# Kernel tuning notes

Measured on AMD Instinct MI355X. Metric: run time of the kernel, lower is better.

The kernel has to match this reference:

```python
import jax, jax.numpy as jnp
import numpy as np

N = 160000   # active voxels
C = 64       # embed_channels
K = 2048     # clusters per level
G = 128      # voxel grid side (grid_size)
NEG = 0.01   # LeakyReLU negative slope (torch default)
EPS_BN = 1e-5


def _build_neighbors():
    # Random unique active voxels in a G^3 grid; 27-neighborhood index map for SubMConv3d.
    rng = np.random.default_rng(0)
    codes = np.sort(rng.choice(G ** 3, size=N, replace=False))
    xc = codes // (G * G); yc = (codes // G) % G; zc = codes % G
    nbrs = []
    for dx in (-1, 0, 1):
        for dy in (-1, 0, 1):
            for dz in (-1, 0, 1):
                nx, ny, nz = xc + dx, yc + dy, zc + dz
                inb = (nx >= 0) & (nx < G) & (ny >= 0) & (ny < G) & (nz >= 0) & (nz < G)
                ncode = nx * (G * G) + ny * G + nz
                pos = np.searchsorted(codes, np.where(inb, ncode, 0))
                pos = np.clip(pos, 0, N - 1)
                found = inb & (codes[pos] == ncode)
                nbrs.append(np.where(found, pos, -1))
    return np.stack(nbrs).astype(np.int32)  # [27, N], -1 = no active neighbor


def setup_inputs():
    key = jax.random.key(0)
    def nrm(i, shape, s=0.05):
        return jax.random.normal(jax.random.fold_in(key, i), shape, jnp.float32) * s
    return {
        'feat': jax.random.normal(jax.random.fold_in(key, 0), (N, C), jnp.float32),
        'lw_W': nrm(1, (3, C, C)), 'lw_g': jnp.ones((3, C)), 'lw_b': jnp.zeros((3, C)),
        'w_W': nrm(2, (3, C, C)),
        'proj_W': nrm(3, (4, C, C)), 'proj_g': jnp.ones((4, C)), 'proj_b': jnp.zeros((4, C)),
        'adaptive_W': nrm(4, (C, 3)),
        'fuse_W': nrm(5, (2 * C, C)), 'fuse_g': jnp.ones((C,)), 'fuse_b': jnp.zeros((C,)),
        'conv1_W': nrm(6, (27, C, C)), 'bn1_g': jnp.ones((C,)), 'bn1_b': jnp.zeros((C,)),
        'conv2_W': nrm(7, (27, C, C)), 'bn2_g': jnp.ones((C,)), 'bn2_b': jnp.zeros((C,)),
        'clusters': jax.random.randint(jax.random.fold_in(key, 8), (3, N), 0, K, dtype=jnp.int32),
        'nbr': jnp.asarray(_build_neighbors()),
    }


def _bn(x, g, b):
    # BatchNorm1d, training-mode (biased batch stats over N)
    m = x.mean(0)
    v = x.var(0)
    return (x - m) * jax.lax.rsqrt(v + EPS_BN) * g + b


def _lrelu(x):
    return jax.nn.leaky_relu(x, NEG)


def _seg_sum(x, seg):
    return jax.ops.segment_sum(x, seg, num_segments=K)


def _subm_conv(f, nbr, W):
    # Submanifold 3x3x3 conv: per kernel offset, masked gather + [C,C] matmul.
    out = jnp.zeros((f.shape[0], W.shape[-1]), f.dtype)
    for k in range(27):
        idx = nbr[k]
        g = jnp.where((idx >= 0)[:, None], f[jnp.maximum(idx, 0)], 0.0)
        out = out + g @ W[k]
    return out


def reference(feat, lw_W, lw_g, lw_b, w_W, proj_W, proj_g, proj_b, adaptive_W,
              fuse_W, fuse_g, fuse_b, conv1_W, bn1_g, bn1_b, conv2_W, bn2_g, bn2_b,
              clusters, nbr):
    feats = []
    for i in range(3):  # depth-1 cluster levels
        c = clusters[i]
        cnt = jnp.clip(_seg_sum(jnp.ones((feat.shape[0], 1), feat.dtype), c), 1.0, None)
        pw = _lrelu(_bn(feat @ lw_W[i], lw_g[i], lw_b[i]))
        pw = pw - (_seg_sum(pw, c) / cnt)[c]          # center by cluster mean
        pw = pw @ w_W[i]
        pw = jnp.exp(pw - pw.max())                    # global-max-stabilized exp
        pw = pw / (_seg_sum(pw, c)[c] + 1e-6)          # per-cluster softmax
        pfeat = _lrelu(_bn(feat @ proj_W[i], proj_g[i], proj_b[i])) * pw
        feats.append(_seg_sum(pfeat, c)[c])            # pool then broadcast back
    adp = jax.nn.softmax(feat @ adaptive_W, axis=1)    # [N, 3]
    feats = jnp.stack(feats, axis=1)                   # [N, 3, C]
    feats = jnp.einsum('ln,lnc->lc', adp, feats)
    f = _lrelu(_bn(feat @ proj_W[3], proj_g[3], proj_b[3]))
    f = jnp.concatenate([f, feats], axis=1)
    f = _lrelu(_bn(f @ fuse_W, fuse_g, fuse_b)) + feat
    res = f
    v = _lrelu(_bn(_subm_conv(f, nbr, conv1_W), bn1_g, bn1_b))
    v = _bn(_subm_conv(v, nbr, conv2_W), bn2_g, bn2_b)
    return _lrelu(v + res)
```

## Files before the change

### kernel.cpp

```cpp
#include <hip/hip_runtime.h>
#include <hip/hip_bf16.h>
#include <math.h>

#define KCL 2048
#define LRELU_NEG 0.01f
#define EPSBN 1e-5f
#define OSTR 72

using s8v = __attribute__((ext_vector_type(8))) short;
using f4v = __attribute__((ext_vector_type(4))) float;

union U8 { ushort u[8]; uint4 v; };

__device__ __forceinline__ float lrelu(float x) { return x > 0.f ? x : LRELU_NEG * x; }
__device__ __forceinline__ ushort f2bf(float f) {
    __hip_bfloat16 h = __float2bfloat16(f);
    return *reinterpret_cast<ushort*>(&h);
}
__device__ __forceinline__ float bf2f(ushort u) { return __uint_as_float(((unsigned)u) << 16); }

__device__ __forceinline__ unsigned encf(float f) {
    unsigned u = __float_as_uint(f);
    return (u & 0x80000000u) ? ~u : (u | 0x80000000u);
}
// ... 19 lines not shown
__device__ __forceinline__ void mfma_tileG(const uint4* As, const ushort* Wmat, int ws, int koff,
                                           int rowA0, int rowA1, int swA0, int swA1,
                                           int l15, int lg, f4v acc[2][4]) {
    const s8v* Av = (const s8v*)As;
#pragma unroll
    for (int kb = 0; kb < 2; ++kb) {
        int gch = kb * 4 + lg;
        s8v a0 = Av[rowA0 * 8 + (gch ^ swA0)];
        s8v a1 = Av[rowA1 * 8 + (gch ^ swA1)];
#pragma unroll
        for (int nf = 0; nf < 4; ++nf) {
            int col = nf * 16 + l15;
            s8v bf = *(const s8v*)(Wmat + (size_t)col * ws + koff + gch * 8);
            acc[0][nf] = __builtin_amdgcn_mfma_f32_16x16x32_bf16(a0, bf, acc[0][nf], 0, 0, 0);
            acc[1][nf] = __builtin_amdgcn_mfma_f32_16x16x32_bf16(a1, bf, acc[1][nf], 0, 0, 0);
        }
    }
}

__device__ __forceinline__ void stage_a_bf16(const ushort* S, uint4* As, int row, int n, int arow, int ah) {
    uint4 c0 = {0, 0, 0, 0}, c1 = c0, c2 = c0, c3 = c0;
    if (row < n) {
        const uint4* s = (const uint4*)(S + (size_t)row * 64) + ah * 4;
        c0 = s[0]; c1 = s[1]; c2 = s[2]; c3 = s[3];
    }
    int sw = arow & 7;
    uint4* dst = As + arow * 8;
    dst[(ah * 4 + 0) ^ sw] = c0;
    dst[(ah * 4 + 1) ^ sw] = c1;
    dst[(ah * 4 + 2) ^ sw] = c2;
    dst[(ah * 4 + 3) ^ sw] = c3;
}

__device__ __forceinline__ void stage_a_vals(const float* vals, uint4* As, int arow, int ah) {
    int sw = arow & 7;
    uint4* dst = As + arow * 8;
#pragma unroll
    for (int c = 0; c < 4; ++c) {
        U8 u;
#pragma unroll
        for (int e = 0; e < 8; ++e) u.u[e] = f2bf(vals[c * 8 + e]);
        dst[(ah * 4 + c) ^ sw] = u.v;
    }
}

__device__ __forceinline__ void tile_to_ost(const f4v acc[2][4], ushort* ost, int w, int lane) {
    const int l15 = lane & 15, lg = lane >> 4;
#pragma unroll
    for (int rf = 0; rf < 2; ++rf)
#pragma unroll
        for (int nf = 0; nf < 4; ++nf)
#pragma unroll
            for (int q = 0; q < 4; ++q)
                ost[(w * 32 + rf * 16 + lg * 4 + q) * OSTR + nf * 16 + l15] = f2bf(acc[rf][nf][q]);
}

__device__ __forceinline__ void ost_store(const ushort* ost, ushort* out, int n, int rb, int arow, int ah) {
    int row = rb + arow;
    if (row < n) {
        uint4* dst = (uint4*)(out + (size_t)row * 64 + ah * 32);
        const uint4* src = (const uint4*)(ost + arow * OSTR + ah * 32);
        dst[0] = src[0]; dst[1] = src[1]; dst[2] = src[2]; dst[3] = src[3];
    }
}

__device__ __forceinline__ void tile_stats(const f4v acc[2][4], float* red, double* statp,
                                           int n, int rb, int w, int lane, int t) {
    const int l15 = lane & 15, lg = lane >> 4;
    int base = rb + w * 32;
#pragma unroll
    for (int nf = 0; nf < 4; ++nf) {
        float s = 0.f, s2 = 0.f;
#pragma unroll
        for (int rf = 0; rf < 2; ++rf)
#pragma unroll
            for (int q = 0; q < 4; ++q) {
                int r = base + rf * 16 + lg * 4 + q;
                if (r < n) {
                    float v = acc[rf][nf][q];
                    s += v;
                    s2 += v * v;
                }
            }
        s += __shfl_xor(s, 16); s += __shfl_xor(s, 32);
        s2 += __shfl_xor(s2, 16); s2 += __shfl_xor(s2, 32);
        if (lg == 0) {
            red[w * 64 + nf * 16 + l15] = s;
// ... 89 lines not shown
    int t = threadIdx.x;
    int base = t * 8;
    int v[8];
    int s = 0;
#pragma unroll
    for (int j = 0; j < 8; ++j) { v[j] = c[base + j]; s += v[j]; }
    part[t] = s;
    __syncthreads();
    if (t == 0) {
        int acc = 0;
        for (int i = 0; i < 256; ++i) { pref[i] = acc; acc += part[i]; }
    }
    __syncthreads();
    int acc = pref[t] + l * n;
#pragma unroll
    for (int j = 0; j < 8; ++j) {
        off[l * KCL + base + j] = acc;
        cursor[l * KCL + base + j] = acc;
        acc += v[j];
    }
}

__global__ __launch_bounds__(256) void scatter_kernel(const int* __restrict__ clusters, int* __restrict__ cursor,
                                                      int* __restrict__ perm, int n) {
    long n3 = (long)n * 3;
    for (long i = (long)blockIdx.x * 256 + threadIdx.x; i < n3; i += (long)gridDim.x * 256) {
        int l = (i >= n) + (i >= 2 * (long)n);
        int c = clusters[i];
        int pos = atomicAdd(&cursor[l * KCL + c], 1);
        perm[pos] = (int)(i - (long)l * n);
    }
}

__device__ __forceinline__ void mega_one(const uint4* As, float* red, ushort* ost, const ushort* Wmat,
                                         ushort* out, double* statp, int n, int rb, int w, int lane,
                                         int arow, int ah, int t) {
    const int l15 = lane & 15, lg = lane >> 4;
    int rowA0 = w * 32 + l15, rowA1 = rowA0 + 16;
    f4v acc[2][4];
#pragma unroll
    for (int rf = 0; rf < 2; ++rf)
#pragma unroll
        for (int nf = 0; nf < 4; ++nf)
#pragma unroll
            for (int q = 0; q < 4; ++q) acc[rf][nf][q] = 0.f;
    mfma_tileG(As, Wmat, 64, 0, rowA0, rowA1, rowA0 & 7, rowA1 & 7, l15, lg, acc);
    tile_to_ost(acc, ost, w, lane);
    tile_stats(acc, red, statp, n, rb, w, lane, t);
    __syncthreads();
    ost_store(ost, out, n, rb, arow, ah);
    tile_stats_final(red, statp, t);
    __syncthreads();
}

__global__ __launch_bounds__(256) void mega7_gemm(const ushort* __restrict__ feat16,
                                                  const ushort* __restrict__ wt64,
                                                  ushort* __restrict__ o0, ushort* __restrict__ o1,
                                                  ushort* __restrict__ o2, ushort* __restrict__ o3,
                                                  ushort* __restrict__ o4, ushort* __restrict__ o5,
                                                  ushort* __restrict__ o6,
                                                  int n, double* __restrict__ stats) {
    __shared__ uint4 As[128 * 8];
    __shared__ float red[512];
    __shared__ ushort ost[128 * OSTR];
    int t = threadIdx.x, lane = t & 63, w = t >> 6;
    int rb = blockIdx.x * 128;
    int arow = t >> 1, ah = t & 1;
    stage_a_bf16(feat16, As, rb + arow, n, arow, ah);
    __syncthreads();
    mega_one(As, red, ost, wt64 + (size_t)0 * 4096, o0, stats + 0 * 128, n, rb, w, lane, arow, ah, t);
    mega_one(As, red, ost, wt64 + (size_t)1 * 4096, o1, stats + 2 * 128, n, rb, w, lane, arow, ah, t);
    mega_one(As, red, ost, wt64 + (size_t)2 * 4096, o2, stats + 4 * 128, n, rb, w, lane, arow, ah, t);
    mega_one(As, red, ost, wt64 + (size_t)6 * 4096, o3, stats + 1 * 128, n, rb, w, lane, arow, ah, t);
    mega_one(As, red, ost, wt64 + (size_t)7 * 4096, o4, stats + 3 * 128, n, rb, w, lane, arow, ah, t);
    mega_one(As, red, ost, wt64 + (size_t)8 * 4096, o5, stats + 5 * 128, n, rb, w, lane, arow, ah, t);
    mega_one(As, red, ost, wt64 + (size_t)9 * 4096, o6, stats + 6 * 128, n, rb, w, lane, arow, ah, t);
}

__global__ __launch_bounds__(256) void reduce_mean3_kernel(const ushort* __restrict__ A3,
                                                           const double* __restrict__ stats,
                                                           const float* __restrict__ lw_g,
                                                           const float* __restrict__ lw_b, int n,
                                                           const int* __restrict__ cnts, const int* __restrict__ offs,
                                                           const int* __restrict__ perm,
                                                           float* __restrict__ meanB3) {
    int l = blockIdx.x >> 11, c = blockIdx.x & (KCL - 1);
    const ushort* A = A3 + (size_t)l * n * 64;
    __shared__ float sb[128];
    bn_sb(stats + (size_t)(2 * l) * 128, lw_g + l * 64, lw_b + l * 64, n, sb);
    int t = threadIdx.x, col = t & 63, rg = t >> 6;
    int o = offs[l * KCL + c], m = cnts[l * KCL + c];
    float acc = 0.f;
    float sc = sb[col], bi = sb[64 + col];
    for (int j = rg; j < m; j += 4) {
        int row = perm[o + j];
        acc += lrelu(bf2f(A[(size_t)row * 64 + col]) * sc + bi);
    }
    __shared__ float red[256];
    red[t] = acc;
    __syncthreads();
    if (t < 64) {
        float s = red[t] + red[t + 64] + red[t + 128] + red[t + 192];
        float cf = (float)m;
        if (cf < 1.f) cf = 1.f;
        meanB3[(size_t)l * KCL * 64 + (size_t)c * 64 + col] = s / cf;
    }
}

__global__ __launch_bounds__(256) void mw3_gemm(const float* __restrict__ meanB3, const ushort* __restrict__ wW16,
                                                float* __restrict__ MW3) {
    __shared__ uint4 As[128 * 8];
    int l = blockIdx.x >> 4, b = blockIdx.x & 15;
    const float* src = meanB3 + (size_t)l * KCL * 64;
    float* out = MW3 + (size_t)l * KCL * 64;
    int t = threadIdx.x, lane = t & 63, w = t >> 6;
    int rb = b * 128;
    int arow = t >> 1, ah = t & 1;
    const int l15 = lane & 15, lg = lane >> 4;
    {
        float vals[32];
        const float4* s = (const float4*)(src + (size_t)(rb + arow) * 64 + ah * 32);
#pragma unroll
        for (int q = 0; q < 8; ++q) {
            float4 x = s[q];
            vals[q * 4 + 0] = x.x; vals[q * 4 + 1] = x.y;
            vals[q * 4 + 2] = x.z; vals[q * 4 + 3] = x.w;
        }
        stage_a_vals(vals, As, arow, ah);
    }
    __syncthreads();
    f4v acc[2][4];
#pragma unroll
    for (int rf = 0; rf < 2; ++rf)
#pragma unroll
        for (int nf = 0; nf < 4; ++nf)
#pragma unroll
            for (int q = 0; q < 4; ++q) acc[rf][nf][q] = 0.f;
    int rowA0 = w * 32 + l15, rowA1 = rowA0 + 16;
    mfma_tileG(As, wW16 + (size_t)l * 4096, 64, 0, rowA0, rowA1, rowA0 & 7, rowA1 & 7, l15, lg, acc);
    int base = rb + w * 32;
#pragma unroll
    for (int rf = 0; rf < 2; ++rf)
#pragma unroll
        for (int nf = 0; nf < 4; ++nf)
#pragma unroll
            for (int q = 0; q < 4; ++q) {
                int r = base + rf * 16 + lg * 4 + q;
                out[(size_t)r * 64 + nf * 16 + l15] = acc[rf][nf][q];
            }
}

__global__ __launch_bounds__(256) void cgemm3(ushort* __restrict__ A3io, const ushort* __restrict__ wW16,
                                              const float* __restrict__ MW3, const int* __restrict__ clusters,
                                              const double* __restrict__ stats, const float* __restrict__ lw_g,
                                              const float* __restrict__ lw_b,
                                              unsigned* __restrict__ gmax, int n, int nb) {
    __shared__ uint4 As[128 * 8];
    __shared__ float sb[128];
    __shared__ ushort ost[128 * OSTR];
    int l = blockIdx.x / nb, b = blockIdx.x % nb;
    ushort* A = A3io + (size_t)l * n * 64;
    const float* MW = MW3 + (size_t)l * KCL * 64;
    const int* clus = clusters + (size_t)l * n;
    int t = threadIdx.x, lane = t & 63, w = t >> 6;
    int rb = b * 128;
    int arow = t >> 1, ah = t & 1;
    const int l15 = lane & 15, lg = lane >> 4;

    bn_sb(stats + (size_t)(2 * l) * 128, lw_g + l * 64, lw_b + l * 64, n, sb);
    {
        int row = rb + arow;
        float vals[32];
        if (row < n) {
            const U8* s8p = (const U8*)(A + (size_t)row * 64 + ah * 32);
#pragma unroll
            for (int c = 0; c < 4; ++c) {
                U8 u = s8p[c];
#pragma unroll
                for (int e = 0; e < 8; ++e) {
                    int col = ah * 32 + c * 8 + e;
                    vals[c * 8 + e] = lrelu(bf2f(u.u[e]) * sb[col] + sb[64 + col]);
                }
            }
        } else {
#pragma unroll
            for (int i = 0; i < 32; ++i) vals[i] = 0.f;
        }
        stage_a_vals(vals, As, arow, ah);
    }
    __syncthreads();
    f4v acc[2][4];
#pragma unroll
    for (int rf = 0; rf < 2; ++rf)
#pragma unroll
        for (int nf = 0; nf < 4; ++nf)
#pragma unroll
            for (int q = 0; q < 4; ++q) acc[rf][nf][q] = 0.f;
    int rowA0 = w * 32 + l15, rowA1 = rowA0 + 16;
    mfma_tileG(As, wW16 + (size_t)l * 4096, 64, 0, rowA0, rowA1, rowA0 & 7, rowA1 & 7, l15, lg, acc);
    int base = rb + w * 32;
    float m = -INFINITY;
#pragma unroll
    for (int rf = 0; rf < 2; ++rf)
#pragma unroll
        for (int q = 0; q < 4; ++q) {
            int r = base + rf * 16 + lg * 4 + q;
            int c = (r < n) ? clus[r] : 0;
            const float* mwr = MW + (size_t)c * 64;
            int orow = (w * 32 + rf * 16 + lg * 4 + q) * OSTR;
#pragma unroll
            for (int nf = 0; nf < 4; ++nf) {
                int col = nf * 16 + l15;
                float v = acc[rf][nf][q] - mwr[col];
                ost[orow + col] = f2bf(v);
                if (r < n) m = fmaxf(m, v);
            }
        }
    float* sp = (float*)As;
    sp[t] = m;
    __syncthreads();
    ost_store(ost, A, n, rb, arow, ah);
    for (int s = 128; s > 0; s >>= 1) {
        if (t < s) sp[t] = fmaxf(sp[t], sp[t + s]);
        __syncthreads();
    }
    if (t == 0) atomicMax(&gmax[l], encf(sp[0]));
}

__global__ __launch_bounds__(256) void expf3_kernel(const ushort* __restrict__ C3, const ushort* __restrict__ E0,
                                                    const ushort* __restrict__ E1, const ushort* __restrict__ E2,
                                                    const double* __restrict__ stats,
                                                    const float* __restrict__ proj_g, const float* __restrict__ proj_b,
                                                    int n, const unsigned* __restrict__ gmax,
                                                    const int* __restrict__ cnts, const int* __restrict__ offs,
                                                    const int* __restrict__ perm, float* __restrict__ seg3) {
    int l = blockIdx.x >> 11, c = blockIdx.x & (KCL - 1);
    const ushort* C = C3 + (size_t)l * n * 64;
    const ushort* E = (l == 0) ? E0 : (l == 1) ? E1 : E2;
    __shared__ float sb[128];
    bn_sb(stats + (size_t)(2 * l + 1) * 128, proj_g + l * 64, proj_b + l * 64, n, sb);
    int t = threadIdx.x, col = t & 63, rg = t >> 6;
    float gm = decf(gmax[l]);
    int o = offs[l * KCL + c], m = cnts[l * KCL + c];
    float accd = 0.f, accn = 0.f;
    float sc = sb[col], bi = sb[64 + col];
    for (int j = rg; j < m; j += 4) {
        int row = perm[o + j];
        float d = expf(bf2f(C[(size_t)row * 64 + col]) - gm);
        float pf = lrelu(bf2f(E[(size_t)row * 64 + col]) * sc + bi);
        accd += d;
        accn += pf * d;
    }
    __shared__ float redd[256], redn[256];
    redd[t] = accd;
    redn[t] = accn;
    __syncthreads();
    if (t < 64) {
        float sd = redd[t] + redd[t + 64] + redd[t + 128] + redd[t + 192];
        float sn = redn[t] + redn[t + 64] + redn[t + 128] + redn[t + 192];
        seg3[(size_t)l * KCL * 64 + (size_t)c * 64 + col] = sn / (sd + 1e-6f);
    }
}

__global__ __launch_bounds__(256) void fuse_mfma(const ushort* __restrict__ P3, const double* __restrict__ statsP,
                                                 const float* __restrict__ gg, const float* __restrict__ bb, int n,
                                                 const float* __restrict__ adp, const int* __restrict__ clusters,
                                                 const float* __restrict__ s3_0, const float* __restrict__ s3_1,
                                                 const float* __restrict__ s3_2, const ushort* __restrict__ WfT,
                                                 ushort* __restrict__ out, double* __restrict__ stats_out) {
    __shared__ uint4 As[128 * 8];
    __shared__ float sb[128];
    __shared__ ushort ost[128 * OSTR];
    int t = threadIdx.x, lane = t & 63, w = t >> 6;
    int rb = blockIdx.x * 128;
    int arow = t >> 1, ah = t & 1;
    const int l15 = lane & 15, lg = lane >> 4;

    bn_sb(statsP, gg, bb, n, sb);

    f4v acc[2][4];
#pragma unroll
    for (int rf = 0; rf < 2; ++rf)
#pragma unroll
        for (int nf = 0; nf < 4; ++nf)
#pragma unroll
            for (int q = 0; q < 4; ++q) acc[rf][nf][q] = 0.f;

    int rowA0 = w * 32 + l15, rowA1 = rowA0 + 16;
    int row = rb + arow;

    for (int p = 0; p < 2; ++p) {
        if (p) __syncthreads();
        float vals[32];
        if (row < n) {
            if (p == 0) {
                const U8* s8p = (const U8*)(P3 + (size_t)row * 64 + ah * 32);
#pragma unroll
                for (int c = 0; c < 4; ++c) {
                    U8 u = s8p[c];
#pragma unroll
                    for (int e = 0; e < 8; ++e) {
                        int col = ah * 32 + c * 8 + e;
                        vals[c * 8 + e] = lrelu(bf2f(u.u[e]) * sb[col] + sb[64 + col]);
                    }
                }
            } else {
                float a0 = adp[(size_t)row * 3 + 0], a1 = adp[(size_t)row * 3 + 1], a2 = adp[(size_t)row * 3 + 2];
                const float* r0 = s3_0 + (size_t)clusters[row] * 64 + ah * 32;
                const float* r1 = s3_1 + (size_t)clusters[(size_t)n + row] * 64 + ah * 32;
                const float* r2 = s3_2 + (size_t)clusters[2 * (size_t)n + row] * 64 + ah * 32;
#pragma unroll
                for (int i = 0; i < 32; ++i) vals[i] = a0 * r0[i] + a1 * r1[i] + a2 * r2[i];
            }
        } else {
#pragma unroll
            for (int i = 0; i < 32; ++i) vals[i] = 0.f;
        }
        stage_a_vals(vals, As, arow, ah);
        __syncthreads();
        mfma_tileG(As, WfT, 128, p * 64, rowA0, rowA1, rowA0 & 7, rowA1 & 7, l15, lg, acc);
    }
    tile_to_ost(acc, ost, w, lane);
    float* red = (float*)As;
    tile_stats(acc, red, stats_out, n, rb, w, lane, t);
    __syncthreads();
    ost_store(ost, out, n, rb, arow, ah);
    tile_stats_final(red, stats_out, t);
}

__global__ __launch_bounds__(256) void subm_conv_db(const ushort* __restrict__ fin, const int* __restrict__ nbr,
                                                    const ushort* __restrict__ Wt, ushort* __restrict__ vout,
                                                    int n, double* __restrict__ stats_out) {
    __shared__ uint4 As[2][128 * 8];
    __shared__ uint4 Ws[2][64 * 8];
    int t = threadIdx.x;
    int lane = t & 63, w = t >> 6;
    int rb = blockIdx.x * 128;
    int arow = t >> 1, ah = t & 1;
    int wrow = t >> 2, wq = t & 3;
    const int l15 = lane & 15, lg = lane >> 4;
    int rowA0 = w * 32 + l15, rowA1 = rowA0 + 16;
    int swA0 = rowA0 & 7, swA1 = rowA1 & 7;
    const bool rowok = (rb + arow) < n;
    const int swa = arow & 7, sww = wrow & 7;

    f4v acc[2][4];
#pragma unroll
    for (int rf = 0; rf < 2; ++rf)
#pragma unroll
        for (int nf = 0; nf < 4; ++nf)
#pragma unroll
            for (int q = 0; q < 4; ++q) acc[rf][nf][q] = 0.f;

    bool fc0, fc1, wzc, wzn = false;
    {
        int gi = rowok ? nbr[rb + arow] : -1;
// ... 54 lines not shown
                    s8v av0 = Av[rowA0 * 8 + (gch ^ swA0)];
#pragma unroll
                    for (int nf = 0; nf < 4; ++nf)
                        acc[0][nf] = __builtin_amdgcn_mfma_f32_16x16x32_bf16(av0, bfr[nf], acc[0][nf], 0, 0, 0);
                }
                if (fc1) {
                    s8v av1 = Av[rowA1 * 8 + (gch ^ swA1)];
#pragma unroll
                    for (int nf = 0; nf < 4; ++nf)
                        acc[1][nf] = __builtin_amdgcn_mfma_f32_16x16x32_bf16(av1, bfr[nf], acc[1][nf], 0, 0, 0);
                }
            }
        }
        if (k < 26) {
            if (!(missn && wzn)) {
                uint4* dst = As[cur ^ 1] + arow * 8;
                dst[(ah * 4 + 0) ^ swa] = a0;
                dst[(ah * 4 + 1) ^ swa] = a1;
                dst[(ah * 4 + 2) ^ swa] = a2;
                dst[(ah * 4 + 3) ^ swa] = a3;
            }
            uint4* wdst = Ws[cur ^ 1] + wrow * 8;
            wdst[wq ^ sww] = w0;
            wdst[(wq + 4) ^ sww] = w1;
            cur ^= 1;
            bool nw = wzc;
            wzc = missn;
            wzn = nw;
            fc0 = fn0;
            fc1 = fn1;
        }
    }
    __syncthreads();
    ushort* ost = (ushort*)As;
    float* red = (float*)Ws;
    tile_to_ost(acc, ost, w, lane);
    tile_stats(acc, red, stats_out, n, rb, w, lane, t);
    __syncthreads();
    ost_store(ost, vout, n, rb, arow, ah);
    tile_stats_final(red, stats_out, t);
}

__global__ __launch_bounds__(256) void addfeat_kernel(const ushort* __restrict__ t3, const double* __restrict__ stats,
                                                      const float* __restrict__ g, const float* __restrict__ b,
                                                      const float* __restrict__ feat, ushort* __restrict__ f16,
                                                      int n) {
    __shared__ float sb[128];
    bn_sb(stats, g, b, n, sb);
    long total4 = (long)n * 16;
    for (long i = (long)blockIdx.x * 256 + threadIdx.x; i < total4; i += (long)gridDim.x * 256) {
        int c0 = (int)(i & 15) * 4;
        ushort4 xv = ((const ushort4*)t3)[i];
        float4 fz = ((const float4*)feat)[i];
        ushort4 u;
        u.x = f2bf(lrelu(bf2f(xv.x) * sb[c0 + 0] + sb[64 + c0 + 0]) + fz.x);
        u.y = f2bf(lrelu(bf2f(xv.y) * sb[c0 + 1] + sb[64 + c0 + 1]) + fz.y);
        u.z = f2bf(lrelu(bf2f(xv.z) * sb[c0 + 2] + sb[64 + c0 + 2]) + fz.z);
        u.w = f2bf(lrelu(bf2f(xv.w) * sb[c0 + 3] + sb[64 + c0 + 3]) + fz.w);
        ((ushort4*)f16)[i] = u;
    }
}

__global__ __launch_bounds__(256) void bnlrelu_tobf16_kernel(const ushort* __restrict__ v,
                                                             const double* __restrict__ stats,
                                                             const float* __restrict__ g, const float* __restrict__ b,
                                                             ushort* __restrict__ o16, int n) {
    __shared__ float sb[128];
    bn_sb(stats, g, b, n, sb);
// ... 66 lines not shown
    size_t stats_off = alloc((size_t)10 * 128 * 8);
    size_t gmax_off = alloc(16);
    size_t zbytes = off;
    size_t offs_off = alloc((size_t)3 * KCL * 4);
    size_t cur_off = alloc((size_t)3 * KCL * 4);
    size_t perm_off = alloc((size_t)3 * n * 4);
    size_t mean_off = alloc((size_t)3 * KCL * 64 * 4);
    size_t mw_off = alloc((size_t)3 * KCL * 64 * 4);
    size_t seg3_off = alloc((size_t)3 * KCL * 64 * 4);
    size_t adp_off = alloc((size_t)n * 3 * 4);
    size_t feat16_off = alloc((size_t)n * 64 * 2);
    size_t ra_off = alloc((size_t)3 * n * 64 * 2);
    size_t re_off = alloc((size_t)2 * n * 64 * 2);
    size_t wt64_off = alloc((size_t)64 * 4096 * 2);
    size_t wfT_off = alloc((size_t)8192 * 2);

    int* cnts = (int*)(ws + cnt_off);
    double* stats = (double*)(ws + stats_off);
    unsigned* gmax = (unsigned*)(ws + gmax_off);
    int* offs = (int*)(ws + offs_off);
    int* cursor = (int*)(ws + cur_off);
    int* perm = (int*)(ws + perm_off);
    float* meanB3 = (float*)(ws + mean_off);
    float* MW3 = (float*)(ws + mw_off);
    float* seg3 = (float*)(ws + seg3_off);
    float* adp = (float*)(ws + adp_off);
    ushort* feat16 = (ushort*)(ws + feat16_off);
    ushort* RA = (ushort*)(ws + ra_off);
    ushort* RE = (ushort*)(ws + re_off);
    ushort* wt64 = (ushort*)(ws + wt64_off);
    ushort* wfT = (ushort*)(ws + wfT_off);
    float* outp = (float*)d_out;

    ushort* A3 = RA;
    ushort* E0 = RE;
    ushort* E1 = RE + (size_t)n * 64;
    ushort* E2 = (ushort*)d_out;
    ushort* P3 = (ushort*)d_out + (size_t)n * 64;
    ushort* t3buf = RA;
    ushort* fbuf16 = RA + (size_t)n * 64;
    ushort* c1out = RA + (size_t)2 * n * 64;
    ushort* cbuf = RE;
    ushort* c2out = RE + (size_t)n * 64;

    const ushort* wW16 = wt64 + (size_t)3 * 4096;
    const ushort* conv1W16 = wt64 + (size_t)10 * 4096;
    const ushort* conv2W16 = wt64 + (size_t)37 * 4096;

    hipMemsetAsync(d_ws, 0, zbytes, stream);

    const int GEMM_BLK = (n + 127) / 128;
    const int EW_BLK = 2048;

    prep_wt64<<<64, 256, 0, stream>>>(lw_W, w_W, proj_W, conv1_W, conv2_W, wt64);
    prep_fuse<<<1, 256, 0, stream>>>(fuse_W, wfT);
    adp_cvt_kernel<<<1024, 256, 0, stream>>>(feat, adaptive_W, adp, feat16, n);

    hist3_kernel<<<384, 256, 0, stream>>>(clusters, cnts, n);
    scan_kernel<<<3, 256, 0, stream>>>(cnts, offs, cursor, n);
    scatter_kernel<<<1024, 256, 0, stream>>>(clusters, cursor, perm, n);

    mega7_gemm<<<GEMM_BLK, 256, 0, stream>>>(feat16, wt64,
                                             A3, A3 + (size_t)n * 64, A3 + (size_t)2 * n * 64,
                                             E0, E1, E2, P3, n, stats);
    reduce_mean3_kernel<<<3 * KCL, 256, 0, stream>>>(A3, stats, lw_g, lw_b, n, cnts, offs, perm, meanB3);
    mw3_gemm<<<3 * 16, 256, 0, stream>>>(meanB3, wW16, MW3);
    cgemm3<<<3 * GEMM_BLK, 256, 0, stream>>>(A3, wW16, MW3, clusters, stats, lw_g, lw_b, gmax, n, GEMM_BLK);
    expf3_kernel<<<3 * KCL, 256, 0, stream>>>(A3, E0, E1, E2, stats, proj_g, proj_b, n, gmax,
                                              cnts, offs, perm, seg3);

    fuse_mfma<<<GEMM_BLK, 256, 0, stream>>>(P3, stats + 6 * 128, proj_g + 192, proj_b + 192, n,
                                            adp, clusters,
                                            seg3, seg3 + (size_t)KCL * 64, seg3 + (size_t)2 * KCL * 64,
                                            wfT, t3buf, stats + 7 * 128);
    addfeat_kernel<<<EW_BLK, 256, 0, stream>>>(t3buf, stats + 7 * 128, fuse_g, fuse_b, feat, fbuf16, n);

    subm_conv_db<<<GEMM_BLK, 256, 0, stream>>>(fbuf16, nbr, conv1W16, c1out, n, stats + 8 * 128);
    bnlrelu_tobf16_kernel<<<EW_BLK, 256, 0, stream>>>(c1out, stats + 8 * 128, bn1_g, bn1_b, cbuf, n);

    subm_conv_db<<<GEMM_BLK, 256, 0, stream>>>(cbuf, nbr, conv2W16, c2out, n, stats + 9 * 128);
    final_kernel<<<EW_BLK, 256, 0, stream>>>(c2out, stats + 9 * 128, bn2_g, bn2_b, fbuf16, outp, n);
}
```

Baseline: 589.6 us.

## Recompute projection GEMMs on the fly instead of materializing seven intermediate tensors

The first GEMM kernel now only accumulates batch-norm statistics for the seven projections and no longer writes the bf16 outputs. Every downstream kernel (cluster mean, global max, per-cluster softmax/pool, fuse) recomputes its projection from feat16 with MFMA, gathering rows via the cluster permutation where needed. This removes large intermediate writes and reads to global memory, at the cost of redundant matrix multiplies and extra shared-memory staging in the cluster-gather kernels.

```diff
diff --git a/kernel.cpp b/kernel.cpp
--- a/kernel.cpp
+++ b/kernel.cpp
@@ -75,6 +75,20 @@
     dst[(ah * 4 + 3) ^ sw] = c3;
 }
 
+__device__ __forceinline__ void stage_a_gather(const ushort* S, uint4* As, int gi, int arow, int ah) {
+    uint4 c0 = {0, 0, 0, 0}, c1 = c0, c2 = c0, c3 = c0;
+    if (gi >= 0) {
+        const uint4* s = (const uint4*)(S + (size_t)gi * 64) + ah * 4;
+        c0 = s[0]; c1 = s[1]; c2 = s[2]; c3 = s[3];
+    }
+    int sw = arow & 7;
+    uint4* dst = As + arow * 8;
+    dst[(ah * 4 + 0) ^ sw] = c0;
+    dst[(ah * 4 + 1) ^ sw] = c1;
+    dst[(ah * 4 + 2) ^ sw] = c2;
+    dst[(ah * 4 + 3) ^ sw] = c3;
+}
+
 __device__ __forceinline__ void stage_a_vals(const float* vals, uint4* As, int arow, int ah) {
     int sw = arow & 7;
     uint4* dst = As + arow * 8;
@@ -96,6 +110,17 @@
 #pragma unroll
             for (int q = 0; q < 4; ++q)
                 ost[(w * 32 + rf * 16 + lg * 4 + q) * OSTR + nf * 16 + l15] = f2bf(acc[rf][nf][q]);
+}
+
+__device__ __forceinline__ void ost_read_row(const ushort* ost, int arow, int ah, float* vals) {
+    const uint4* src = (const uint4*)(ost + arow * OSTR + ah * 32);
+#pragma unroll
+    for (int c = 0; c < 4; ++c) {
+        U8 u;
+        u.v = src[c];
+#pragma unroll
+        for (int e = 0; e < 8; ++e) vals[c * 8 + e] = bf2f(u.u[e]);
+    }
 }
 
 __device__ __forceinline__ void ost_store(const ushort* ost, ushort* out, int n, int rb, int arow, int ah) {
@@ -251,78 +276,96 @@
     }
 }
 
-__device__ __forceinline__ void mega_one(const uint4* As, float* red, ushort* ost, const ushort* Wmat,
-                                         ushort* out, double* statp, int n, int rb, int w, int lane,
-                                         int arow, int ah, int t) {
-    const int l15 = lane & 15, lg = lane >> 4;
-    int rowA0 = w * 32 + l15, rowA1 = rowA0 + 16;
-    f4v acc[2][4];
-#pragma unroll
-    for (int rf = 0; rf < 2; ++rf)
-#pragma unroll
-        for (int nf = 0; nf < 4; ++nf)
-#pragma unroll
-            for (int q = 0; q < 4; ++q) acc[rf][nf][q] = 0.f;
-    mfma_tileG(As, Wmat, 64, 0, rowA0, rowA1, rowA0 & 7, rowA1 & 7, l15, lg, acc);
-    tile_to_ost(acc, ost, w, lane);
-    tile_stats(acc, red, statp, n, rb, w, lane, t);
-    __syncthreads();
-    ost_store(ost, out, n, rb, arow, ah);
-    tile_stats_final(red, statp, t);
-    __syncthreads();
-}
-
-__global__ __launch_bounds__(256) void mega7_gemm(const ushort* __restrict__ feat16,
-                                                  const ushort* __restrict__ wt64,
-                                                  ushort* __restrict__ o0, ushort* __restrict__ o1,
-                                                  ushort* __restrict__ o2, ushort* __restrict__ o3,
-                                                  ushort* __restrict__ o4, ushort* __restrict__ o5,
-                                                  ushort* __restrict__ o6,
-                                                  int n, double* __restrict__ stats) {
+__global__ __launch_bounds__(256) void stats7_gemm(const ushort* __restrict__ feat16,
+                                                   const ushort* __restrict__ wt64,
+                                                   int n, double* __restrict__ stats) {
     __shared__ uint4 As[128 * 8];
     __shared__ float red[512];
-    __shared__ ushort ost[128 * OSTR];
     int t = threadIdx.x, lane = t & 63, w = t >> 6;
     int rb = blockIdx.x * 128;
     int arow = t >> 1, ah = t & 1;
+    const int l15 = lane & 15, lg = lane >> 4;
+    int rowA0 = w * 32 + l15, rowA1 = rowA0 + 16;
     stage_a_bf16(feat16, As, rb + arow, n, arow, ah);
     __syncthreads();
-    mega_one(As, red, ost, wt64 + (size_t)0 * 4096, o0, stats + 0 * 128, n, rb, w, lane, arow, ah, t);
-    mega_one(As, red, ost, wt64 + (size_t)1 * 4096, o1, stats + 2 * 128, n, rb, w, lane, arow, ah, t);
-    mega_one(As, red, ost, wt64 + (size_t)2 * 4096, o2, stats + 4 * 128, n, rb, w, lane, arow, ah, t);
-    mega_one(As, red, ost, wt64 + (size_t)6 * 4096, o3, stats + 1 * 128, n, rb, w, lane, arow, ah, t);
-    mega_one(As, red, ost, wt64 + (size_t)7 * 4096, o4, stats + 3 * 128, n, rb, w, lane, arow, ah, t);
-    mega_one(As, red, ost, wt64 + (size_t)8 * 4096, o5, stats + 5 * 128, n, rb, w, lane, arow, ah, t);
-    mega_one(As, red, ost, wt64 + (size_t)9 * 4096, o6, stats + 6 * 128, n, rb, w, lane, arow, ah, t);
-}
-
-__global__ __launch_bounds__(256) void reduce_mean3_kernel(const ushort* __restrict__ A3,
-                                                           const double* __restrict__ stats,
-                                                           const float* __restrict__ lw_g,
-                                                           const float* __restrict__ lw_b, int n,
-                                                           const int* __restrict__ cnts, const int* __restrict__ offs,
-                                                           const int* __restrict__ perm,
-                                                           float* __restrict__ meanB3) {
+    const int wsl[7] = {0, 1, 2, 6, 7, 8, 9};
+    const int ssl[7] = {0, 2, 4, 1, 3, 5, 6};
+#pragma unroll
+    for (int p = 0; p < 7; ++p) {
+        f4v acc[2][4];
+#pragma unroll
+        for (int rf = 0; rf < 2; ++rf)
+#pragma unroll
+            for (int nf = 0; nf < 4; ++nf)
+#pragma unroll
+                for (int q = 0; q < 4; ++q) acc[rf][nf][q] = 0.f;
+        mfma_tileG(As, wt64 + (size_t)wsl[p] * 4096, 64, 0, rowA0, rowA1, rowA0 & 7, rowA1 & 7,
+                   l15, lg, acc);
+        tile_stats(acc, red, stats + (size_t)ssl[p] * 128, n, rb, w, lane, t);
+        __syncthreads();
+        tile_stats_final(red, stats + (size_t)ssl[p] * 128, t);
+        __syncthreads();
+    }
+}
+
+__global__ __launch_bounds__(256) void mean3_fused(const ushort* __restrict__ feat16,
+                                                   const ushort* __restrict__ wt64,
+                                                   const double* __restrict__ stats,
+                                                   const float* __restrict__ lw_g, const float* __restrict__ lw_b,
+                                                   int n, const int* __restrict__ cnts,
+                                                   const int* __restrict__ offs, const int* __restrict__ perm,
+                                                   float* __restrict__ meanB3) {
     int l = blockIdx.x >> 11, c = blockIdx.x & (KCL - 1);
-    const ushort* A = A3 + (size_t)l * n * 64;
     __shared__ float sb[128];
+    __shared__ uint4 As[128 * 8];
+    __shared__ float red[256];
     bn_sb(stats + (size_t)(2 * l) * 128, lw_g + l * 64, lw_b + l * 64, n, sb);
-    int t = threadIdx.x, col = t & 63, rg = t >> 6;
+    int t = threadIdx.x, lane = t & 63, w = t >> 6;
+    int arow = t >> 1, ah = t & 1;
+    const int l15 = lane & 15, lg = lane >> 4;
+    int rowA0 = w * 32 + l15, rowA1 = rowA0 + 16;
+    const ushort* Wm = wt64 + (size_t)l * 4096;
     int o = offs[l * KCL + c], m = cnts[l * KCL + c];
-    float acc = 0.f;
-    float sc = sb[col], bi = sb[64 + col];
-    for (int j = rg; j < m; j += 4) {
-        int row = perm[o + j];
-        acc += lrelu(bf2f(A[(size_t)row * 64 + col]) * sc + bi);
-    }
-    __shared__ float red[256];
-    red[t] = acc;
+    float colsum[4] = {0.f, 0.f, 0.f, 0.f};
+    for (int ch = 0; ch < m; ch += 128) {
+        int j = ch + arow;
+        int gi = (j < m) ? perm[o + j] : -1;
+        __syncthreads();
+        stage_a_gather(feat16, As, gi, arow, ah);
+        __syncthreads();
+        f4v acc[2][4];
+#pragma unroll
+        for (int rf = 0; rf < 2; ++rf)
+#pragma unroll
+            for (int nf = 0; nf < 4; ++nf)
+#pragma unroll
+                for (int q = 0; q < 4; ++q) acc[rf][nf][q] = 0.f;
+        mfma_tileG(As, Wm, 64, 0, rowA0, rowA1, rowA0 & 7, rowA1 & 7, l15, lg, acc);
+#pragma unroll
+        for (int rf = 0; rf < 2; ++rf)
+#pragma unroll
+            for (int q = 0; q < 4; ++q) {
+                int jr = ch + w * 32 + rf * 16 + lg * 4 + q;
+                if (jr < m)
+#pragma unroll
+                    for (int nf = 0; nf < 4; ++nf) {
+                        int col = nf * 16 + l15;
+                        colsum[nf] += lrelu(acc[rf][nf][q] * sb[col] + sb[64 + col]);
+                    }
+            }
+    }
+#pragma unroll
+    for (int nf = 0; nf < 4; ++nf) {
+        float s = colsum[nf];
+        s += __shfl_xor(s, 16); s += __shfl_xor(s, 32);
+        if (lg == 0) red[w * 64 + nf * 16 + l15] = s;
+    }
     __syncthreads();
     if (t < 64) {
-        float s = red[t] + red[t + 64] + red[t + 128] + red[t + 192];
+        float s = red[t] + red[64 + t] + red[128 + t] + red[192 + t];
         float cf = (float)m;
         if (cf < 1.f) cf = 1.f;
-        meanB3[(size_t)l * KCL * 64 + (size_t)c * 64 + col] = s / cf;
+        meanB3[((size_t)l * KCL + c) * 64 + t] = s / cf;
     }
 }
 
@@ -369,76 +412,77 @@
             }
 }
 
-__global__ __launch_bounds__(256) void cgemm3(ushort* __restrict__ A3io, const ushort* __restrict__ wW16,
-                                              const float* __restrict__ MW3, const int* __restrict__ clusters,
-                                              const double* __restrict__ stats, const float* __restrict__ lw_g,
-                                              const float* __restrict__ lw_b,
-                                              unsigned* __restrict__ gmax, int n, int nb) {
+__global__ __launch_bounds__(256) void gmax3_kernel(const ushort* __restrict__ feat16,
+                                                    const ushort* __restrict__ wt64,
+                                                    const float* __restrict__ MW3,
+                                                    const int* __restrict__ clusters,
+                                                    const double* __restrict__ stats,
+                                                    const float* __restrict__ lw_g, const float* __restrict__ lw_b,
+                                                    unsigned* __restrict__ gmax, int n, int nb) {
+    __shared__ float sb[128];
     __shared__ uint4 As[128 * 8];
-    __shared__ float sb[128];
+    __shared__ uint4 As2[128 * 8];
     __shared__ ushort ost[128 * OSTR];
+    __shared__ float sp[256];
     int l = blockIdx.x / nb, b = blockIdx.x % nb;
-    ushort* A = A3io + (size_t)l * n * 64;
-    const float* MW = MW3 + (size_t)l * KCL * 64;
-    const int* clus = clusters + (size_t)l * n;
+    int rb = b * 128;
+    bn_sb(stats + (size_t)(2 * l) * 128, lw_g + l * 64, lw_b + l * 64, n, sb);
     int t = threadIdx.x, lane = t & 63, w = t >> 6;
-    int rb = b * 128;
     int arow = t >> 1, ah = t & 1;
     const int l15 = lane & 15, lg = lane >> 4;
-
-    bn_sb(stats + (size_t)(2 * l) * 128, lw_g + l * 64, lw_b + l * 64, n, sb);
+    int rowA0 = w * 32 + l15, rowA1 = rowA0 + 16;
+    const int* clus = clusters + (size_t)l * n;
+
+    stage_a_bf16(feat16, As, rb + arow, n, arow, ah);
+    __syncthreads();
+    f4v accA[2][4];
+#pragma unroll
+    for (int rf = 0; rf < 2; ++rf)
+#pragma unroll
+        for (int nf = 0; nf < 4; ++nf)
+#pragma unroll
+            for (int q = 0; q < 4; ++q) accA[rf][nf][q] = 0.f;
+    mfma_tileG(As, wt64 + (size_t)l * 4096, 64, 0, rowA0, rowA1, rowA0 & 7, rowA1 & 7, l15, lg, accA);
+    tile_to_ost(accA, ost, w, lane);
+    __syncthreads();
     {
-        int row = rb + arow;
         float vals[32];
-        if (row < n) {
-            const U8* s8p = (const U8*)(A + (size_t)row * 64 + ah * 32);
-#pragma unroll
-            for (int c = 0; c < 4; ++c) {
-                U8 u = s8p[c];
-#pragma unroll
-                for (int e = 0; e < 8; ++e) {
-                    int col = ah * 32 + c * 8 + e;
-                    vals[c * 8 + e] = lrelu(bf2f(u.u[e]) * sb[col] + sb[64 + col]);
+        ost_read_row(ost, arow, ah, vals);
+#pragma unroll
+        for (int i = 0; i < 32; ++i) {
+            int col = ah * 32 + i;
+            vals[i] = lrelu(vals[i] * sb[col] + sb[64 + col]);
+        }
+        stage_a_vals(vals, As2, arow, ah);
+    }
+    __syncthreads();
+    f4v accC[2][4];
+#pragma unroll
+    for (int rf = 0; rf < 2; ++rf)
+#pragma unroll
+        for (int nf = 0; nf < 4; ++nf)
+#pragma unroll
+            for (int q = 0; q < 4; ++q) accC[rf][nf][q] = 0.f;
+    mfma_tileG(As2, wt64 + (size_t)(3 + l) * 4096, 64, 0, rowA0, rowA1, rowA0 & 7, rowA1 & 7,
+               l15, lg, accC);
+    float mx = -INFINITY;
+#pragma unroll
+    for (int rf = 0; rf < 2; ++rf)
+#pragma unroll
+        for (int q = 0; q < 4; ++q) {
+            int r = rb + w * 32 + rf * 16 + lg * 4 + q;
+            if (r < n) {
+                int cc = clus[r];
+                const float* mwr = MW3 + ((size_t)l * KCL + cc) * 64;
+#pragma unroll
+                for (int nf = 0; nf < 4; ++nf) {
+                    int col = nf * 16 + l15;
+                    mx = fmaxf(mx, accC[rf][nf][q] - mwr[col]);
                 }
             }
-        } else {
-#pragma unroll
-            for (int i = 0; i < 32; ++i) vals[i] = 0.f;
-        }
-        stage_a_vals(vals, As, arow, ah);
-    }
-    __syncthreads();
-    f4v acc[2][4];
-#pragma unroll
-    for (int rf = 0; rf < 2; ++rf)
-#pragma unroll
-        for (int nf = 0; nf < 4; ++nf)
-#pragma unroll
-            for (int q = 0; q < 4; ++q) acc[rf][nf][q] = 0.f;
-    int rowA0 = w * 32 + l15, rowA1 = rowA0 + 16;
-    mfma_tileG(As, wW16 + (size_t)l * 4096, 64, 0, rowA0, rowA1, rowA0 & 7, rowA1 & 7, l15, lg, acc);
-    int base = rb + w * 32;
-    float m = -INFINITY;
-#pragma unroll
-    for (int rf = 0; rf < 2; ++rf)
-#pragma unroll
-        for (int q = 0; q < 4; ++q) {
-            int r = base + rf * 16 + lg * 4 + q;
-            int c = (r < n) ? clus[r] : 0;
-            const float* mwr = MW + (size_t)c * 64;
-            int orow = (w * 32 + rf * 16 + lg * 4 + q) * OSTR;
-#pragma unroll
-            for (int nf = 0; nf < 4; ++nf) {
-                int col = nf * 16 + l15;
-                float v = acc[rf][nf][q] - mwr[col];
-                ost[orow + col] = f2bf(v);
-                if (r < n) m = fmaxf(m, v);
-            }
-        }
-    float* sp = (float*)As;
-    sp[t] = m;
-    __syncthreads();
-    ost_store(ost, A, n, rb, arow, ah);
+        }
+    sp[t] = mx;
+    __syncthreads();
     for (int s = 128; s > 0; s >>= 1) {
         if (t < s) sp[t] = fmaxf(sp[t], sp[t + s]);
         __syncthreads();
@@ -446,101 +490,178 @@
     if (t == 0) atomicMax(&gmax[l], encf(sp[0]));
 }
 
-__global__ __launch_bounds__(256) void expf3_kernel(const ushort* __restrict__ C3, const ushort* __restrict__ E0,
-                                                    const ushort* __restrict__ E1, const ushort* __restrict__ E2,
-                                                    const double* __restrict__ stats,
-                                                    const float* __restrict__ proj_g, const float* __restrict__ proj_b,
-                                                    int n, const unsigned* __restrict__ gmax,
-                                                    const int* __restrict__ cnts, const int* __restrict__ offs,
-                                                    const int* __restrict__ perm, float* __restrict__ seg3) {
+__global__ __launch_bounds__(256) void seg3_fused(const ushort* __restrict__ feat16,
+                                                  const ushort* __restrict__ wt64,
+                                                  const float* __restrict__ MW3,
+                                                  const double* __restrict__ stats,
+                                                  const float* __restrict__ lw_g, const float* __restrict__ lw_b,
+                                                  const float* __restrict__ proj_g, const float* __restrict__ proj_b,
+                                                  int n, const unsigned* __restrict__ gmax,
+                                                  const int* __restrict__ cnts, const int* __restrict__ offs,
+                                                  const int* __restrict__ perm, float* __restrict__ seg3) {
     int l = blockIdx.x >> 11, c = blockIdx.x & (KCL - 1);
-    const ushort* C = C3 + (size_t)l * n * 64;
-    const ushort* E = (l == 0) ? E0 : (l == 1) ? E1 : E2;
-    __shared__ float sb[128];
-    bn_sb(stats + (size_t)(2 * l + 1) * 128, proj_g + l * 64, proj_b + l * 64, n, sb);
-    int t = threadIdx.x, col = t & 63, rg = t >> 6;
+    __shared__ float sbA[128], sbE[128];
+    __shared__ uint4 As[128 * 8];
+    __shared__ uint4 As2[128 * 8];
+    __shared__ ushort ost[128 * OSTR];
+    __shared__ float redd[256], redn[256];
+    bn_sb(stats + (size_t)(2 * l) * 128, lw_g + l * 64, lw_b + l * 64, n, sbA);
+    bn_sb(stats + (size_t)(2 * l + 1) * 128, proj_g + l * 64, proj_b + l * 64, n, sbE);
+    int t = threadIdx.x, lane = t & 63, w = t >> 6;
+    int arow = t >> 1, ah = t & 1;
+    const int l15 = lane & 15, lg = lane >> 4;
+    int rowA0 = w * 32 + l15, rowA1 = rowA0 + 16;
     float gm = decf(gmax[l]);
     int o = offs[l * KCL + c], m = cnts[l * KCL + c];
-    float accd = 0.f, accn = 0.f;
-    float sc = sb[col], bi = sb[64 + col];
-    for (int j = rg; j < m; j += 4) {
-        int row = perm[o + j];
-        float d = expf(bf2f(C[(size_t)row * 64 + col]) - gm);
-        float pf = lrelu(bf2f(E[(size_t)row * 64 + col]) * sc + bi);
-        accd += d;
-        accn += pf * d;
-    }
-    __shared__ float redd[256], redn[256];
-    redd[t] = accd;
-    redn[t] = accn;
+    const ushort* WmL = wt64 + (size_t)l * 4096;
+    const ushort* WmW = wt64 + (size_t)(3 + l) * 4096;
+    const ushort* WmP = wt64 + (size_t)(6 + l) * 4096;
+    float mwv[4];
+#pragma unroll
+    for (int nf = 0; nf < 4; ++nf)
+        mwv[nf] = MW3[((size_t)l * KCL + c) * 64 + nf * 16 + l15];
+    float accd[4] = {0.f, 0.f, 0.f, 0.f}, accn[4] = {0.f, 0.f, 0.f, 0.f};
+
+    for (int ch = 0; ch < m; ch += 128) {
+        int j = ch + arow;
+        int gi = (j < m) ? perm[o + j] : -1;
+        __syncthreads();
+        stage_a_gather(feat16, As, gi, arow, ah);
+        __syncthreads();
+        f4v accA[2][4], accE[2][4];
+#pragma unroll
+        for (int rf = 0; rf < 2; ++rf)
+#pragma unroll
+            for (int nf = 0; nf < 4; ++nf)
+#pragma unroll
+                for (int q = 0; q < 4; ++q) { accA[rf][nf][q] = 0.f; accE[rf][nf][q] = 0.f; }
+        mfma_tileG(As, WmL, 64, 0, rowA0, rowA1, rowA0 & 7, rowA1 & 7, l15, lg, accA);
+        mfma_tileG(As, WmP, 64, 0, rowA0, rowA1, rowA0 & 7, rowA1 & 7, l15, lg, accE);
+        tile_to_ost(accA, ost, w, lane);
+        __syncthreads();
+        {
+            float vals[32];
+            ost_read_row(ost, arow, ah, vals);
+#pragma unroll
+            for (int i = 0; i < 32; ++i) {
+                int col = ah * 32 + i;
+                vals[i] = lrelu(vals[i] * sbA[col] + sbA[64 + col]);
+            }
+            stage_a_vals(vals, As2, arow, ah);
+        }
+        __syncthreads();
+        f4v accC[2][4];
+#pragma unroll
+        for (int rf = 0; rf < 2; ++rf)
+#pragma unroll
+            for (int nf = 0; nf < 4; ++nf)
+#pragma unroll
+                for (int q = 0; q < 4; ++q) accC[rf][nf][q] = 0.f;
+        mfma_tileG(As2, WmW, 64, 0, rowA0, rowA1, rowA0 & 7, rowA1 & 7, l15, lg, accC);
+#pragma unroll
+        for (int rf = 0; rf < 2; ++rf)
+#pragma unroll
+            for (int q = 0; q < 4; ++q) {
+                int jr = ch + w * 32 + rf * 16 + lg * 4 + q;
+                if (jr < m)
+#pragma unroll
+                    for (int nf = 0; nf < 4; ++nf) {
+                        int col = nf * 16 + l15;
+                        float d = expf(accC[rf][nf][q] - mwv[nf] - gm);
+                        float pf = lrelu(accE[rf][nf][q] * sbE[col] + sbE[64 + col]);
+                        accd[nf] += d;
+                        accn[nf] += pf * d;
+                    }
+            }
+    }
+#pragma unroll
+    for (int nf = 0; nf < 4; ++nf) {
+        float s = accd[nf], s2 = accn[nf];
+        s += __shfl_xor(s, 16); s += __shfl_xor(s, 32);
+        s2 += __shfl_xor(s2, 16); s2 += __shfl_xor(s2, 32);
+        if (lg == 0) {
+            redd[w * 64 + nf * 16 + l15] = s;
+            redn[w * 64 + nf * 16 + l15] = s2;
+        }
+    }
     __syncthreads();
     if (t < 64) {
-        float sd = redd[t] + redd[t + 64] + redd[t + 128] + redd[t + 192];
-        float sn = redn[t] + redn[t + 64] + redn[t + 128] + redn[t + 192];
-        seg3[(size_t)l * KCL * 64 + (size_t)c * 64 + col] = sn / (sd + 1e-6f);
-    }
-}
-
-__global__ __launch_bounds__(256) void fuse_mfma(const ushort* __restrict__ P3, const double* __restrict__ statsP,
+        float sd = redd[t] + redd[64 + t] + redd[128 + t] + redd[192 + t];
+        float sn = redn[t] + redn[64 + t] + redn[128 + t] + redn[192 + t];
+        seg3[((size_t)l * KCL + c) * 64 + t] = sn / (sd + 1e-6f);
+    }
+}
+
+__global__ __launch_bounds__(256) void fuse_mfma(const ushort* __restrict__ feat16,
+                                                 const ushort* __restrict__ wt64,
+                                                 const double* __restrict__ statsP,
                                                  const float* __restrict__ gg, const float* __restrict__ bb, int n,
                                                  const float* __restrict__ adp, const int* __restrict__ clusters,
                                                  const float* __restrict__ s3_0, const float* __restrict__ s3_1,
                                                  const float* __restrict__ s3_2, const ushort* __restrict__ WfT,
                                                  ushort* __restrict__ out, double* __restrict__ stats_out) {
     __shared__ uint4 As[128 * 8];
+    __shared__ uint4 As2[128 * 8];
+    __shared__ ushort ost[128 * OSTR];
     __shared__ float sb[128];
-    __shared__ ushort ost[128 * OSTR];
     int t = threadIdx.x, lane = t & 63, w = t >> 6;
     int rb = blockIdx.x * 128;
     int arow = t >> 1, ah = t & 1;
     const int l15 = lane & 15, lg = lane >> 4;
-
-    bn_sb(statsP, gg, bb, n, sb);
-
-    f4v acc[2][4];
-#pragma unroll
-    for (int rf = 0; rf < 2; ++rf)
-#pragma unroll
-        for (int nf = 0; nf < 4; ++nf)
-#pragma unroll
-            for (int q = 0; q < 4; ++q) acc[rf][nf][q] = 0.f;
-
     int rowA0 = w * 32 + l15, rowA1 = rowA0 + 16;
     int row = rb + arow;
 
-    for (int p = 0; p < 2; ++p) {
-        if (p) __syncthreads();
-        float vals[32];
+    bn_sb(statsP, gg, bb, n, sb);
+    stage_a_bf16(feat16, As, row, n, arow, ah);
+    __syncthreads();
+
+    f4v accP[2][4];
+#pragma unroll
+    for (int rf = 0; rf < 2; ++rf)
+#pragma unroll
+        for (int nf = 0; nf < 4; ++nf)
+#pragma unroll
+            for (int q = 0; q < 4; ++q) accP[rf][nf][q] = 0.f;
+    mfma_tileG(As, wt64 + (size_t)9 * 4096, 64, 0, rowA0, rowA1, rowA0 & 7, rowA1 & 7, l15, lg, accP);
+    tile_to_ost(accP, ost, w, lane);
+    __syncthreads();
+    {
+        float pv[32];
+        ost_read_row(ost, arow, ah, pv);
+#pragma unroll
+        for (int i = 0; i < 32; ++i) {
+            int col = ah * 32 + i;
+            pv[i] = lrelu(pv[i] * sb[col] + sb[64 + col]);
+        }
+        stage_a_vals(pv, As2, arow, ah);
+        float bv[32];
         if (row < n) {
-            if (p == 0) {
-                const U8* s8p = (const U8*)(P3 + (size_t)row * 64 + ah * 32);
-#pragma unroll
-                for (int c = 0; c < 4; ++c) {
-                    U8 u = s8p[c];
-#pragma unroll
-                    for (int e = 0; e < 8; ++e) {
-                        int col = ah * 32 + c * 8 + e;
-                        vals[c * 8 + e] = lrelu(bf2f(u.u[e]) * sb[col] + sb[64 + col]);
-                    }
-                }
-            } else {
-                float a0 = adp[(size_t)row * 3 + 0], a1 = adp[(size_t)row * 3 + 1], a2 = adp[(size_t)row * 3 + 2];
-                const float* r0 = s3_0 + (size_t)clusters[row] * 64 + ah * 32;
-                const float* r1 = s3_1 + (size_t)clusters[(size_t)n + row] * 64 + ah * 32;
-                const float* r2 = s3_2 + (size_t)clusters[2 * (size_t)n + row] * 64 + ah * 32;
-#pragma unroll
-                for (int i = 0; i < 32; ++i) vals[i] = a0 * r0[i] + a1 * r1[i] + a2 * r2[i];
-            }
+            float a0 = adp[(size_t)row * 3 + 0], a1 = adp[(size_t)row * 3 + 1], a2 = adp[(size_t)row * 3 + 2];
+            const float* r0 = s3_0 + (size_t)clusters[row] * 64 + ah * 32;
+            const float* r1 = s3_1 + (size_t)clusters[(size_t)n + row] * 64 + ah * 32;
+            const float* r2 = s3_2 + (size_t)clusters[2 * (size_t)n + row] * 64 + ah * 32;
+#pragma unroll
+            for (int i = 0; i < 32; ++i) bv[i] = a0 * r0[i] + a1 * r1[i] + a2 * r2[i];
         } else {
 #pragma unroll
-            for (int i = 0; i < 32; ++i) vals[i] = 0.f;
-        }
-        stage_a_vals(vals, As, arow, ah);
-        __syncthreads();
-        mfma_tileG(As, WfT, 128, p * 64, rowA0, rowA1, rowA0 & 7, rowA1 & 7, l15, lg, acc);
-    }
+            for (int i = 0; i < 32; ++i) bv[i] = 0.f;
+        }
+        stage_a_vals(bv, As, arow, ah);
+    }
+    __syncthreads();
+
+    f4v acc[2][4];
+#pragma unroll
+    for (int rf = 0; rf < 2; ++rf)
+#pragma unroll
+        for (int nf = 0; nf < 4; ++nf)
+#pragma unroll
+            for (int q = 0; q < 4; ++q) acc[rf][nf][q] = 0.f;
+    mfma_tileG(As2, WfT, 128, 0, rowA0, rowA1, rowA0 & 7, rowA1 & 7, l15, lg, acc);
+    mfma_tileG(As, WfT, 128, 64, rowA0, rowA1, rowA0 & 7, rowA1 & 7, l15, lg, acc);
+    __syncthreads();
+    float* red = (float*)As2;
     tile_to_ost(acc, ost, w, lane);
-    float* red = (float*)As;
     tile_stats(acc, red, stats_out, n, rb, w, lane, t);
     __syncthreads();
     ost_store(ost, out, n, rb, arow, ah);
@@ -661,8 +782,8 @@
         }
     }
     __syncthreads();
-    ushort* ost = (ushort*)As;
-    float* red = (float*)Ws;
+    ushort* ost = (ushort*)As[0];
+    float* red = (float*)Ws[0];
     tile_to_ost(acc, ost, w, lane);
     tile_stats(acc, red, stats_out, n, rb, w, lane, t);
     __syncthreads();
@@ -795,11 +916,6 @@
     ushort* wfT = (ushort*)(ws + wfT_off);
     float* outp = (float*)d_out;
 
-    ushort* A3 = RA;
-    ushort* E0 = RE;
-    ushort* E1 = RE + (size_t)n * 64;
-    ushort* E2 = (ushort*)d_out;
-    ushort* P3 = (ushort*)d_out + (size_t)n * 64;
     ushort* t3buf = RA;
     ushort* fbuf16 = RA + (size_t)n * 64;
     ushort* c1out = RA + (size_t)2 * n * 64;
@@ -823,17 +939,17 @@
     scan_kernel<<<3, 256, 0, stream>>>(cnts, offs, cursor, n);
     scatter_kernel<<<1024, 256, 0, stream>>>(clusters, cursor, perm, n);
 
-    mega7_gemm<<<GEMM_BLK, 256, 0, stream>>>(feat16, wt64,
-                                             A3, A3 + (size_t)n * 64, A3 + (size_t)2 * n * 64,
-                                             E0, E1, E2, P3, n, stats);
-    reduce_mean3_kernel<<<3 * KCL, 256, 0, stream>>>(A3, stats, lw_g, lw_b, n, cnts, offs, perm, meanB3);
+    stats7_gemm<<<GEMM_BLK, 256, 0, stream>>>(feat16, wt64, n, stats);
+    mean3_fused<<<3 * KCL, 256, 0, stream>>>(feat16, wt64, stats, lw_g, lw_b, n, cnts, offs, perm,
+                                             meanB3);
     mw3_gemm<<<3 * 16, 256, 0, stream>>>(meanB3, wW16, MW3);
-    cgemm3<<<3 * GEMM_BLK, 256, 0, stream>>>(A3, wW16, MW3, clusters, stats, lw_g, lw_b, gmax, n, GEMM_BLK);
-    expf3_kernel<<<3 * KCL, 256, 0, stream>>>(A3, E0, E1, E2, stats, proj_g, proj_b, n, gmax,
-                                              cnts, offs, perm, seg3);
-
-    fuse_mfma<<<GEMM_BLK, 256, 0, stream>>>(P3, stats + 6 * 128, proj_g + 192, proj_b + 192, n,
-                                            adp, clusters,
+    gmax3_kernel<<<3 * GEMM_BLK, 256, 0, stream>>>(feat16, wt64, MW3, clusters, stats, lw_g, lw_b,
+                                                   gmax, n, GEMM_BLK);
+    seg3_fused<<<3 * KCL, 256, 0, stream>>>(feat16, wt64, MW3, stats, lw_g, lw_b, proj_g, proj_b,
+                                            n, gmax, cnts, offs, perm, seg3);
+
+    fuse_mfma<<<GEMM_BLK, 256, 0, stream>>>(feat16, wt64, stats + 6 * 128, proj_g + 192, proj_b + 192,
+                                            n, adp, clusters,
                                             seg3, seg3 + (size_t)KCL * 64, seg3 + (size_t)2 * KCL * 64,
                                             wfT, t3buf, stats + 7 * 128);
     addfeat_kernel<<<EW_BLK, 256, 0, stream>>>(t3buf, stats + 7 * 128, fuse_g, fuse_b, feat, fbuf16, n);
```

Result: no change. 601.3 us (+2.0%).
